# Kernel tuning notes

Measured on AMD Instinct MI355X. Metric: run time of the kernel, lower is better.

The kernel has to match this reference:

```python
import jax, jax.numpy as jnp
import numpy as np

N_INST = 50000
D_IN, D_HID, D_ATT = 1024, 512, 256  # size_dict['small']
N_ENS = 4
N_CLS = 2
CB_SIZE = 256
BETA = 0.25
TOP_K = 1


def setup_inputs() -> dict:
    key = jax.random.key(0)
    ks = jax.random.split(key, 9)
    h = jax.random.normal(ks[0], (N_INST, D_IN), dtype=jnp.float32)
    fc_W = jax.random.normal(ks[1], (D_IN, D_HID), dtype=jnp.float32) * (1.0 / np.sqrt(D_IN))
    fc_b = jnp.zeros((D_HID,), dtype=jnp.float32)
    Ua = jax.random.normal(ks[2], (N_ENS, D_HID, D_ATT), dtype=jnp.float32) * (1.0 / np.sqrt(D_HID))
    Ub = jax.random.normal(ks[3], (N_ENS, D_HID, D_ATT), dtype=jnp.float32) * (1.0 / np.sqrt(D_HID))
    Uc = jax.random.normal(ks[4], (N_ENS, D_ATT, 1), dtype=jnp.float32) * (1.0 / np.sqrt(D_ATT))
    cls_W = jax.random.normal(ks[5], (D_HID, N_CLS), dtype=jnp.float32) * (1.0 / np.sqrt(D_HID))
    cls_b = jnp.zeros((N_CLS,), dtype=jnp.float32)
    codebook = jax.random.normal(ks[6], (CB_SIZE, D_HID), dtype=jnp.float32)
    return {"h": h, "fc_W": fc_W, "fc_b": fc_b, "Ua": Ua, "Ub": Ub,
            "Uc": Uc, "cls_W": cls_W, "cls_b": cls_b, "codebook": codebook}


def _vector_quantization(M, codebook):
    # NOTE: original code uses +2*matmul (sign bug in torch source); kept faithful.
    dist = (jnp.sum(M * M, axis=1, keepdims=True)
            + jnp.sum(codebook * codebook, axis=1)
            + 2.0 * (M @ codebook.T))                      # [1, CB]
    inds = jnp.argmin(dist, axis=1)                        # [1]
    one_hot = jax.nn.one_hot(inds, CB_SIZE, dtype=M.dtype)  # [1, CB]
    q = one_hot @ codebook                                  # [1, D_HID]
    commitment = jnp.mean((jax.lax.stop_gradient(q) - M) ** 2)
    embedding = jnp.mean((q - jax.lax.stop_gradient(M)) ** 2)
    vq_loss = commitment * BETA + embedding
    q_st = M + jax.lax.stop_gradient(q - M)  # straight-through (unused downstream)
    return vq_loss, q_st


def reference(h, fc_W, fc_b, Ua, Ub, Uc, cls_W, cls_b, codebook):
    # fc + ReLU: [n, D_HID]
    x = jax.nn.relu(h @ fc_W + fc_b)
    # gated batch-ensemble attention (ensemble dim n=4 broadcast)
    xe = jnp.broadcast_to(x[None], (N_ENS, x.shape[0], D_HID))
    a = jnp.tanh(jnp.einsum('ndk,nkl->ndl', xe, Ua))         # [4, n, D_ATT]
    b = jax.nn.sigmoid(jnp.einsum('ndk,nkl->ndl', xe, Ub))   # [4, n, D_ATT]
    A = jnp.einsum('ndk,nkl->ndl', a * b, Uc).sum(0)          # [n, 1]
    A = jax.nn.sigmoid(A.T)                                   # [1, n]
    M = (A @ x) / jnp.sum(A)                                  # [1, D_HID]
    vq_loss, _M_code = _vector_quantization(M, codebook)
    logits = M @ cls_W + cls_b                                # [1, N_CLS]
    y_probs = jax.nn.softmax(logits, axis=1)
    _, top_idx = jax.lax.top_k(y_probs[:, 1], TOP_K)          # [1]
    top_instance = logits[top_idx]                            # [1, N_CLS]
    Y_hat = jnp.argmax(top_instance, axis=1)[:, None]         # [1, 1] int
    Y_prob = jax.nn.softmax(top_instance, axis=1)
    return (top_instance, Y_prob, Y_hat, vq_loss, y_probs, A)
```

## Files before the change

### kernel.cpp

```cpp
#include <hip/hip_runtime.h>
#include <hip/hip_bf16.h>
#include <math.h>

typedef __bf16 bf16_t;
typedef __bf16 bf16x8 __attribute__((ext_vector_type(8)));
typedef __bf16 bf16x2 __attribute__((ext_vector_type(2)));
typedef float  f32x4  __attribute__((ext_vector_type(4)));

#define MINST 50000

__device__ __forceinline__ float fast_sigmoid(float x){
  return __fdividef(1.f, 1.f + __expf(-x));
}
__device__ __forceinline__ float fast_tanh(float x){
  float e = __expf(2.f*x);
  return 1.f - __fdividef(2.f, e + 1.f);
}

__global__ void prep_wt(const float* __restrict__ W, bf16_t* __restrict__ WT){
  int idx = blockIdx.x*256 + threadIdx.x;
  if (idx >= 512*1024) return;
  int n = idx >> 10, k = idx & 1023;
  WT[idx] = (bf16_t)W[k*512 + n];
}

__global__ void prep_uab(const float* __restrict__ Ua, const float* __restrict__ Ub,
                         bf16_t* __restrict__ UabT){
  int idx = blockIdx.x*256 + threadIdx.x;
  if (idx >= 2048*512) return;
  int c = idx >> 9, k = idx & 511;
  int s = c & 1, t = c >> 1;
  int n = t >> 8, l = t & 255;
  const float* src = s ? Ub : Ua;
  UabT[idx] = (bf16_t)src[(n*512 + k)*256 + l];
}

__global__ void zero_ws_k(float* __restrict__ Alogit, float* __restrict__ Mbuf){
  int i = blockIdx.x*256 + threadIdx.x;
  if (i < MINST) Alogit[i] = 0.f;
  if (i < 513)   Mbuf[i]  = 0.f;
}

template<int EPI, int K>
__global__ __launch_bounds__(256, 2)
void gemm_k(const void* __restrict__ Ap, const bf16_t* __restrict__ Bp, int M,
            const float* __restrict__ bias, bf16_t* __restrict__ Xout,
            const float* __restrict__ Uc, float* __restrict__ Alogit)
{
  __shared__ bf16_t As[128*40] __attribute__((aligned(16)));
  __shared__ bf16_t Bs[128*40] __attribute__((aligned(16)));
  const int tid  = threadIdx.x;
  const int lane = tid & 63;
  const int wid  = tid >> 6;
  const int wr   = wid >> 1;
  const int wc   = wid & 1;
  const int m0   = blockIdx.x * 128;
  const int n0   = blockIdx.y * 128;

  const f32x4 fzero = {0.f, 0.f, 0.f, 0.f};
  f32x4 acc[4][4];
#pragma unroll
  for (int m = 0; m < 4; ++m)
#pragma unroll
    for (int n = 0; n < 4; ++n) acc[m][n] = fzero;

  const int q_row  = tid >> 2;
  const int q_c    = tid & 3;
  const int a_row  = tid >> 1;
  const int a_half = tid & 1;

  bf16x8 sB0, sB1, sA0, sA1;
  f32x4  sAf[4];

  auto loadTiles = [&](int k0){
    sB0 = *(const bf16x8*)(Bp + (size_t)(n0 + q_row     )*K + k0 + q_c*8);
    sB1 = *(const bf16x8*)(Bp + (size_t)(n0 + q_row + 64)*K + k0 + q_c*8);
    if constexpr (EPI == 0) {
      const float* A = (const float*)Ap;
      int gr = m0 + a_row;
      if (gr < M) {
        const f32x4* p = (const f32x4*)(A + (size_t)gr*K + k0 + a_half*16);
        sAf[0]=p[0]; sAf[1]=p[1]; sAf[2]=p[2]; sAf[3]=p[3];
      } else {
        sAf[0]=fzero; sAf[1]=fzero; sAf[2]=fzero; sAf[3]=fzero;
      }
    } else {
      const bf16_t* A = (const bf16_t*)Ap;
      int g0 = m0 + q_row, g1 = m0 + q_row + 64;
      bf16x8 z;
#pragma unroll
      for (int j = 0; j < 8; ++j) z[j] = (bf16_t)0.f;
      sA0 = (g0 < M) ? *(const bf16x8*)(A + (size_t)g0*K + k0 + q_c*8) : z;
      sA1 = (g1 < M) ? *(const bf16x8*)(A + (size_t)g1*K + k0 + q_c*8) : z;
    }
  };

  auto storeTiles = [&](){
    *(bf16x8*)&Bs[(q_row     )*40 + q_c*8] = sB0;
    *(bf16x8*)&Bs[(q_row + 64)*40 + q_c*8] = sB1;
    if constexpr (EPI == 0) {
      bf16x8 lo, hi;
#pragma unroll
      for (int j = 0; j < 4; ++j) {
        lo[j]   = (bf16_t)sAf[0][j];
        lo[4+j] = (bf16_t)sAf[1][j];
        hi[j]   = (bf16_t)sAf[2][j];
        hi[4+j] = (bf16_t)sAf[3][j];
      }
      *(bf16x8*)&As[a_row*40 + a_half*16    ] = lo;
      *(bf16x8*)&As[a_row*40 + a_half*16 + 8] = hi;
    } else {
      *(bf16x8*)&As[(q_row     )*40 + q_c*8] = sA0;
      *(bf16x8*)&As[(q_row + 64)*40 + q_c*8] = sA1;
    }
  };

  loadTiles(0);
  const int fr = lane & 15;
  const int kh = lane >> 4;
  constexpr int NT = K / 32;
  for (int kt = 0; kt < NT; ++kt) {
    __syncthreads();
    storeTiles();
    __syncthreads();
    if (kt + 1 < NT) loadTiles((kt+1)*32);
    bf16x8 a[4], b[4];
#pragma unroll
    for (int m = 0; m < 4; ++m)
      a[m] = *(const bf16x8*)&As[(wr*64 + m*16 + fr)*40 + kh*8];
#pragma unroll
    for (int n = 0; n < 4; ++n)
      b[n] = *(const bf16x8*)&Bs[(wc*64 + n*16 + fr)*40 + kh*8];
#pragma unroll
    for (int m = 0; m < 4; ++m)
#pragma unroll
      for (int n = 0; n < 4; ++n)
        acc[m][n] = __builtin_amdgcn_mfma_f32_16x16x32_bf16(a[m], b[n], acc[m][n], 0, 0, 0);
  }

  const int rg = lane >> 4;
  if constexpr (EPI == 0) {
#pragma unroll
    for (int n = 0; n < 4; ++n) {
      int col = n0 + wc*64 + n*16 + fr;
      float bv = bias[col];
#pragma unroll
      for (int m = 0; m < 4; ++m)
#pragma unroll
        for (int r = 0; r < 4; ++r) {
          int row = m0 + wr*64 + m*16 + rg*4 + r;
          if (row < M) {
            float v = acc[m][n][r] + bv;
            Xout[(size_t)row*512 + col] = (bf16_t)(v > 0.f ? v : 0.f);
          }
        }
    }
  } else {
    float gacc[4][4];
#pragma unroll
    for (int m = 0; m < 4; ++m)
#pragma unroll
      for (int r = 0; r < 4; ++r) gacc[m][r] = 0.f;
    const bool even = (lane & 1) == 0;
#pragma unroll
    for (int n = 0; n < 4; ++n) {
      int col = n0 + wc*64 + n*16 + fr;
      float ucv = Uc[col >> 1];
#pragma unroll
      for (int m = 0; m < 4; ++m)
#pragma unroll
        for (int r = 0; r < 4; ++r) {
          float v = acc[m][n][r];
          float p = __shfl_xor(v, 1);
          float g = even ? fast_tanh(v) * fast_sigmoid(p) * ucv : 0.f;
          gacc[m][r] += g;
        }
    }
#pragma unroll
    for (int m = 0; m < 4; ++m)
#pragma unroll
      for (int r = 0; r < 4; ++r) {
        float s = gacc[m][r];
        s += __shfl_xor(s, 1);
        s += __shfl_xor(s, 2);
        s += __shfl_xor(s, 4);
        s += __shfl_xor(s, 8);
        if (fr == 0) {
          int row = m0 + wr*64 + m*16 + rg*4 + r;
          if (row < M) atomicAdd(&Alogit[row], s);
        }
      }
  }
}

__global__ void a_final(const float* __restrict__ Alogit, float* __restrict__ outA,
                        float* __restrict__ sumA){
  int i = blockIdx.x*256 + threadIdx.x;
  float a = 0.f;
  if (i < MINST) { a = fast_sigmoid(Alogit[i]); outA[i] = a; }
  float s = a;
#pragma unroll
  for (int o = 1; o < 64; o <<= 1) s += __shfl_xor(s, o);
  __shared__ float wsum[4];
  int lane = threadIdx.x & 63, w = threadIdx.x >> 6;
  if (lane == 0) wsum[w] = s;
  __syncthreads();
  if (threadIdx.x == 0) atomicAdd(sumA, wsum[0]+wsum[1]+wsum[2]+wsum[3]);
}

__global__ void m_reduce(const bf16_t* __restrict__ Xb, const float* __restrict__ Aout,
                         float* __restrict__ Mbuf){
  int t = threadIdx.x;
  int c0 = t*2;
  float acc0 = 0.f, acc1 = 0.f;
  for (int r = blockIdx.x; r < MINST; r += gridDim.x) {
    float a = Aout[r];
    bf16x2 x = *(const bf16x2*)(Xb + (size_t)r*512 + c0);
    acc0 += a * (float)x[0];
    acc1 += a * (float)x[1];
  }
  atomicAdd(&Mbuf[c0],   acc0);
  atomicAdd(&Mbuf[c0+1], acc1);
}

__device__ __forceinline__ float block_sum256(float v, float* red){
  int t = threadIdx.x;
  red[t] = v; __syncthreads();
  for (int s = 128; s > 0; s >>= 1) {
    if (t < s) red[t] += red[t+s];
    __syncthreads();
  }
  float r = red[0];
  __syncthreads();
  return r;
}

__global__ __launch_bounds__(256)
void finalize_k(const float* __restrict__ Mbuf, const float* __restrict__ cb,
                const float* __restrict__ clsW, const float* __restrict__ clsb,
                float* __restrict__ dout)
{
  __shared__ float Mn[512];
  __shared__ float red[256];
  __shared__ float dist[256];
  __shared__ int   idxs[256];
  __shared__ int   indS;
  int t = threadIdx.x;
  float sA = Mbuf[512];
  Mn[t]     = Mbuf[t]     / sA;
  Mn[t+256] = Mbuf[t+256] / sA;
  __syncthreads();
  float msq_p = Mn[t]*Mn[t] + Mn[t+256]*Mn[t+256];
  float Msq = block_sum256(msq_p, red);

  const float* cbr = cb + t*512;
  float cs = 0.f, dt = 0.f;
  for (int k = 0; k < 512; k += 4) {
    f32x4 c = *(const f32x4*)(cbr + k);
    cs += c[0]*c[0] + c[1]*c[1] + c[2]*c[2] + c[3]*c[3];
    dt += Mn[k]*c[0] + Mn[k+1]*c[1] + Mn[k+2]*c[2] + Mn[k+3]*c[3];
  }
  dist[t] = Msq + cs + 2.f*dt;
  idxs[t] = t;
  __syncthreads();
  for (int s = 128; s > 0; s >>= 1) {
    if (t < s && dist[t+s] < dist[t]) { dist[t] = dist[t+s]; idxs[t] = idxs[t+s]; }
    __syncthreads();
  }
  if (t == 0) indS = idxs[0];
  __syncthreads();

  const float* q = cb + (size_t)indS*512;
  float d0 = q[t]     - Mn[t];
  float d1 = q[t+256] - Mn[t+256];
  float vqs = block_sum256(d0*d0 + d1*d1, red);
  float vq_loss = 1.25f * (vqs / 512.f);

  float p0 = Mn[t]*clsW[t*2]   + Mn[t+256]*clsW[(t+256)*2];
  float p1 = Mn[t]*clsW[t*2+1] + Mn[t+256]*clsW[(t+256)*2+1];
  float l0 = block_sum256(p0, red);
  float l1 = block_sum256(p1, red);

  if (t == 0) {
    l0 += clsb[0]; l1 += clsb[1];
    float mx = fmaxf(l0, l1);
    float e0 = __expf(l0 - mx), e1 = __expf(l1 - mx);
    float si = e0 + e1;
    float y0 = e0 / si, y1 = e1 / si;
    int yhat = (l1 > l0) ? 1 : 0;
    dout[0] = l0; dout[1] = l1;
    dout[2] = y0; dout[3] = y1;
    dout[4] = (float)yhat;
    dout[5] = vq_loss;
    dout[6] = y0; dout[7] = y1;
  }
}

extern "C" void kernel_launch(void* const* d_in, const int* in_sizes, int n_in,
                              void* d_out, int out_size, void* d_ws, size_t ws_size,
                              hipStream_t stream) {
  const float* h    = (const float*)d_in[0];
  const float* fcW  = (const float*)d_in[1];
  const float* fcb  = (const float*)d_in[2];
  const float* Ua   = (const float*)d_in[3];
  const float* Ub   = (const float*)d_in[4];
  const float* Uc   = (const float*)d_in[5];
  const float* clsW = (const float*)d_in[6];
  const float* clsb = (const float*)d_in[7];
  const float* cbk  = (const float*)d_in[8];
  float* out = (float*)d_out;

  char* ws = (char*)d_ws;
  bf16_t* Xb     = (bf16_t*)ws;
  bf16_t* WT     = (bf16_t*)(ws + 51200000);
  bf16_t* UabT   = (bf16_t*)(ws + 52248576);
  float*  Alogit = (float*)(ws + 54345728);
  float*  Mbuf   = (float*)(ws + 54545728);

  const int M = MINST;

  prep_wt <<<2048, 256, 0, stream>>>(fcW, WT);
  prep_uab<<<4096, 256, 0, stream>>>(Ua, Ub, UabT);
  zero_ws_k<<<196, 256, 0, stream>>>(Alogit, Mbuf);

  gemm_k<0,1024><<<dim3(391, 4), 256, 0, stream>>>(h, WT, M, fcb, Xb, nullptr, nullptr);
  gemm_k<1, 512><<<dim3(391,16), 256, 0, stream>>>(Xb, UabT, M, nullptr, nullptr, Uc, Alogit);

  a_final <<<196, 256, 0, stream>>>(Alogit, out + 8, Mbuf + 512);
  m_reduce<<<256, 256, 0, stream>>>(Xb, out + 8, Mbuf);
  finalize_k<<<1, 256, 0, stream>>>(Mbuf, cbk, clsW, clsb, out);
}
```

Measured before the change: 426.0 us.

## Stage GEMM tiles via global_load_lds double buffering with XCD-aware block remap

```diff
diff --git a/kernel.cpp b/kernel.cpp
--- a/kernel.cpp
+++ b/kernel.cpp
@@ -4,10 +4,15 @@
 
 typedef __bf16 bf16_t;
 typedef __bf16 bf16x8 __attribute__((ext_vector_type(8)));
-typedef __bf16 bf16x2 __attribute__((ext_vector_type(2)));
 typedef float  f32x4  __attribute__((ext_vector_type(4)));
 
 #define MINST 50000
+
+typedef const __attribute__((address_space(1))) void* gas1_t;
+typedef __attribute__((address_space(3))) void* las3_t;
+__device__ __forceinline__ void gload16(const void* g, const void* l){
+  __builtin_amdgcn_global_load_lds((gas1_t)g, (las3_t)l, 16, 0, 0);
+}
 
 __device__ __forceinline__ float fast_sigmoid(float x){
   return __fdividef(1.f, 1.f + __expf(-x));
@@ -41,21 +46,27 @@
   if (i < 513)   Mbuf[i]  = 0.f;
 }
 
-template<int EPI, int K>
+template<int EPI, int K, int NBY>
 __global__ __launch_bounds__(256, 2)
 void gemm_k(const void* __restrict__ Ap, const bf16_t* __restrict__ Bp, int M,
             const float* __restrict__ bias, bf16_t* __restrict__ Xout,
             const float* __restrict__ Uc, float* __restrict__ Alogit)
 {
-  __shared__ bf16_t As[128*40] __attribute__((aligned(16)));
-  __shared__ bf16_t Bs[128*40] __attribute__((aligned(16)));
+  __shared__ bf16_t As[(EPI==0?1:2)][128*32] __attribute__((aligned(16)));
+  __shared__ bf16_t Bs[2][128*32] __attribute__((aligned(16)));
+
   const int tid  = threadIdx.x;
   const int lane = tid & 63;
-  const int wid  = tid >> 6;
-  const int wr   = wid >> 1;
-  const int wc   = wid & 1;
-  const int m0   = blockIdx.x * 128;
-  const int n0   = blockIdx.y * 128;
+  const int w    = tid >> 6;
+  const int wr   = w >> 1;
+  const int wc   = w & 1;
+
+  const int nwg = gridDim.x;
+  const int q = nwg >> 3, r = nwg & 7;
+  const int x = blockIdx.x & 7, pos = blockIdx.x >> 3;
+  const int logical = (x < r ? x*(q+1) : r*(q+1) + (x-r)*q) + pos;
+  const int m0 = (logical / NBY) * 128;
+  const int n0 = (logical % NBY) * 128;
 
   const f32x4 fzero = {0.f, 0.f, 0.f, 0.f};
   f32x4 acc[4][4];
@@ -64,78 +75,97 @@
 #pragma unroll
     for (int n = 0; n < 4; ++n) acc[m][n] = fzero;
 
-  const int q_row  = tid >> 2;
-  const int q_c    = tid & 3;
+  const int srow = lane >> 2;
+  const int schk = (lane & 3) * 8;
+  const bf16_t* bsrc0 = Bp + (size_t)(n0 + w*32 + srow)*K + schk;
+  const bf16_t* bsrc1 = bsrc0 + (size_t)16*K;
+
+  auto stageB = [&](int buf, int k0){
+    gload16(bsrc0 + k0, &Bs[buf][(w*32     )*32]);
+    gload16(bsrc1 + k0, &Bs[buf][(w*32 + 16)*32]);
+  };
+
+  const bf16_t* asrc0 = (const bf16_t*)Ap + (size_t)(m0 + w*32 + srow)*K + schk;
+  const bf16_t* asrc1 = asrc0 + (size_t)16*K;
+  auto stageA1 = [&](int buf, int k0){
+    gload16(asrc0 + k0, &As[buf][(w*32     )*32]);
+    gload16(asrc1 + k0, &As[buf][(w*32 + 16)*32]);
+  };
+
   const int a_row  = tid >> 1;
   const int a_half = tid & 1;
-
-  bf16x8 sB0, sB1, sA0, sA1;
-  f32x4  sAf[4];
-
-  auto loadTiles = [&](int k0){
-    sB0 = *(const bf16x8*)(Bp + (size_t)(n0 + q_row     )*K + k0 + q_c*8);
-    sB1 = *(const bf16x8*)(Bp + (size_t)(n0 + q_row + 64)*K + k0 + q_c*8);
-    if constexpr (EPI == 0) {
-      const float* A = (const float*)Ap;
-      int gr = m0 + a_row;
-      if (gr < M) {
-        const f32x4* p = (const f32x4*)(A + (size_t)gr*K + k0 + a_half*16);
-        sAf[0]=p[0]; sAf[1]=p[1]; sAf[2]=p[2]; sAf[3]=p[3];
-      } else {
-        sAf[0]=fzero; sAf[1]=fzero; sAf[2]=fzero; sAf[3]=fzero;
-      }
+  f32x4 sAf[4];
+  auto loadA0 = [&](int k0){
+    const float* A = (const float*)Ap;
+    int gr = m0 + a_row;
+    if (gr < M) {
+      const f32x4* p = (const f32x4*)(A + (size_t)gr*K + k0 + a_half*16);
+      sAf[0]=p[0]; sAf[1]=p[1]; sAf[2]=p[2]; sAf[3]=p[3];
     } else {
-      const bf16_t* A = (const bf16_t*)Ap;
-      int g0 = m0 + q_row, g1 = m0 + q_row + 64;
-      bf16x8 z;
-#pragma unroll
-      for (int j = 0; j < 8; ++j) z[j] = (bf16_t)0.f;
-      sA0 = (g0 < M) ? *(const bf16x8*)(A + (size_t)g0*K + k0 + q_c*8) : z;
-      sA1 = (g1 < M) ? *(const bf16x8*)(A + (size_t)g1*K + k0 + q_c*8) : z;
+      sAf[0]=fzero; sAf[1]=fzero; sAf[2]=fzero; sAf[3]=fzero;
     }
   };
-
-  auto storeTiles = [&](){
-    *(bf16x8*)&Bs[(q_row     )*40 + q_c*8] = sB0;
-    *(bf16x8*)&Bs[(q_row + 64)*40 + q_c*8] = sB1;
-    if constexpr (EPI == 0) {
-      bf16x8 lo, hi;
-#pragma unroll
-      for (int j = 0; j < 4; ++j) {
-        lo[j]   = (bf16_t)sAf[0][j];
-        lo[4+j] = (bf16_t)sAf[1][j];
-        hi[j]   = (bf16_t)sAf[2][j];
-        hi[4+j] = (bf16_t)sAf[3][j];
-      }
-      *(bf16x8*)&As[a_row*40 + a_half*16    ] = lo;
-      *(bf16x8*)&As[a_row*40 + a_half*16 + 8] = hi;
-    } else {
-      *(bf16x8*)&As[(q_row     )*40 + q_c*8] = sA0;
-      *(bf16x8*)&As[(q_row + 64)*40 + q_c*8] = sA1;
-    }
+  auto writeA0 = [&](){
+    bf16x8 lo, hi;
+#pragma unroll
+    for (int j = 0; j < 4; ++j) {
+      lo[j]   = (bf16_t)sAf[0][j];
+      lo[4+j] = (bf16_t)sAf[1][j];
+      hi[j]   = (bf16_t)sAf[2][j];
+      hi[4+j] = (bf16_t)sAf[3][j];
+    }
+    *(bf16x8*)&As[0][a_row*32 + a_half*16    ] = lo;
+    *(bf16x8*)&As[0][a_row*32 + a_half*16 + 8] = hi;
   };
 
-  loadTiles(0);
   const int fr = lane & 15;
   const int kh = lane >> 4;
   constexpr int NT = K / 32;
-  for (int kt = 0; kt < NT; ++kt) {
-    __syncthreads();
-    storeTiles();
-    __syncthreads();
-    if (kt + 1 < NT) loadTiles((kt+1)*32);
-    bf16x8 a[4], b[4];
-#pragma unroll
-    for (int m = 0; m < 4; ++m)
-      a[m] = *(const bf16x8*)&As[(wr*64 + m*16 + fr)*40 + kh*8];
-#pragma unroll
-    for (int n = 0; n < 4; ++n)
-      b[n] = *(const bf16x8*)&Bs[(wc*64 + n*16 + fr)*40 + kh*8];
-#pragma unroll
-    for (int m = 0; m < 4; ++m)
+
+  if constexpr (EPI == 0) {
+    loadA0(0);
+    stageB(0, 0);
+#pragma unroll 4
+    for (int kt = 0; kt < NT; ++kt) {
+      const int cur = kt & 1;
+      __syncthreads();
+      writeA0();
+      __syncthreads();
+      if (kt + 1 < NT) { loadA0((kt+1)*32); stageB(cur^1, (kt+1)*32); }
+      bf16x8 a[4], b[4];
+#pragma unroll
+      for (int m = 0; m < 4; ++m)
+        a[m] = *(const bf16x8*)&As[0][(wr*64 + m*16 + fr)*32 + kh*8];
 #pragma unroll
       for (int n = 0; n < 4; ++n)
-        acc[m][n] = __builtin_amdgcn_mfma_f32_16x16x32_bf16(a[m], b[n], acc[m][n], 0, 0, 0);
+        b[n] = *(const bf16x8*)&Bs[cur][(wc*64 + n*16 + fr)*32 + kh*8];
+#pragma unroll
+      for (int m = 0; m < 4; ++m)
+#pragma unroll
+        for (int n = 0; n < 4; ++n)
+          acc[m][n] = __builtin_amdgcn_mfma_f32_16x16x32_bf16(a[m], b[n], acc[m][n], 0, 0, 0);
+    }
+  } else {
+    stageA1(0, 0);
+    stageB(0, 0);
+#pragma unroll 4
+    for (int kt = 0; kt < NT; ++kt) {
+      const int cur = kt & 1;
+      __syncthreads();
+      if (kt + 1 < NT) { stageA1(cur^1, (kt+1)*32); stageB(cur^1, (kt+1)*32); }
+      bf16x8 a[4], b[4];
+#pragma unroll
+      for (int m = 0; m < 4; ++m)
+        a[m] = *(const bf16x8*)&As[cur][(wr*64 + m*16 + fr)*32 + kh*8];
+#pragma unroll
+      for (int n = 0; n < 4; ++n)
+        b[n] = *(const bf16x8*)&Bs[cur][(wc*64 + n*16 + fr)*32 + kh*8];
+#pragma unroll
+      for (int m = 0; m < 4; ++m)
+#pragma unroll
+        for (int n = 0; n < 4; ++n)
+          acc[m][n] = __builtin_amdgcn_mfma_f32_16x16x32_bf16(a[m], b[n], acc[m][n], 0, 0, 0);
+    }
   }
 
   const int rg = lane >> 4;
@@ -147,10 +177,10 @@
 #pragma unroll
       for (int m = 0; m < 4; ++m)
 #pragma unroll
-        for (int r = 0; r < 4; ++r) {
-          int row = m0 + wr*64 + m*16 + rg*4 + r;
+        for (int rr = 0; rr < 4; ++rr) {
+          int row = m0 + wr*64 + m*16 + rg*4 + rr;
           if (row < M) {
-            float v = acc[m][n][r] + bv;
+            float v = acc[m][n][rr] + bv;
             Xout[(size_t)row*512 + col] = (bf16_t)(v > 0.f ? v : 0.f);
           }
         }
@@ -160,7 +190,7 @@
 #pragma unroll
     for (int m = 0; m < 4; ++m)
 #pragma unroll
-      for (int r = 0; r < 4; ++r) gacc[m][r] = 0.f;
+      for (int rr = 0; rr < 4; ++rr) gacc[m][rr] = 0.f;
     const bool even = (lane & 1) == 0;
 #pragma unroll
     for (int n = 0; n < 4; ++n) {
@@ -169,25 +199,25 @@
 #pragma unroll
       for (int m = 0; m < 4; ++m)
 #pragma unroll
-        for (int r = 0; r < 4; ++r) {
-          float v = acc[m][n][r];
-          float p = __shfl_xor(v, 1);
-          float g = even ? fast_tanh(v) * fast_sigmoid(p) * ucv : 0.f;
-          gacc[m][r] += g;
+        for (int rr = 0; rr < 4; ++rr) {
+          float v = acc[m][n][rr];
+          float tv = even ? fast_tanh(v) : fast_sigmoid(v);
+          float pv = __shfl_xor(tv, 1);
+          gacc[m][rr] += tv * pv * ucv;
         }
     }
 #pragma unroll
     for (int m = 0; m < 4; ++m)
 #pragma unroll
-      for (int r = 0; r < 4; ++r) {
-        float s = gacc[m][r];
+      for (int rr = 0; rr < 4; ++rr) {
+        float s = gacc[m][rr];
         s += __shfl_xor(s, 1);
         s += __shfl_xor(s, 2);
         s += __shfl_xor(s, 4);
         s += __shfl_xor(s, 8);
         if (fr == 0) {
-          int row = m0 + wr*64 + m*16 + rg*4 + r;
-          if (row < M) atomicAdd(&Alogit[row], s);
+          int row = m0 + wr*64 + m*16 + rg*4 + rr;
+          if (row < M) atomicAdd(&Alogit[row], 0.5f * s);
         }
       }
   }
@@ -211,16 +241,18 @@
 __global__ void m_reduce(const bf16_t* __restrict__ Xb, const float* __restrict__ Aout,
                          float* __restrict__ Mbuf){
   int t = threadIdx.x;
-  int c0 = t*2;
-  float acc0 = 0.f, acc1 = 0.f;
-  for (int r = blockIdx.x; r < MINST; r += gridDim.x) {
+  int c0 = (t & 63) * 8;
+  float acc[8];
+#pragma unroll
+  for (int j = 0; j < 8; ++j) acc[j] = 0.f;
+  for (int r = blockIdx.x*4 + (t>>6); r < MINST; r += gridDim.x*4) {
     float a = Aout[r];
-    bf16x2 x = *(const bf16x2*)(Xb + (size_t)r*512 + c0);
-    acc0 += a * (float)x[0];
-    acc1 += a * (float)x[1];
-  }
-  atomicAdd(&Mbuf[c0],   acc0);
-  atomicAdd(&Mbuf[c0+1], acc1);
+    bf16x8 xv = *(const bf16x8*)(Xb + (size_t)r*512 + c0);
+#pragma unroll
+    for (int j = 0; j < 8; ++j) acc[j] += a * (float)xv[j];
+  }
+#pragma unroll
+  for (int j = 0; j < 8; ++j) atomicAdd(&Mbuf[c0 + j], acc[j]);
 }
 
 __device__ __forceinline__ float block_sum256(float v, float* red){
@@ -230,9 +262,9 @@
     if (t < s) red[t] += red[t+s];
     __syncthreads();
   }
-  float r = red[0];
-  __syncthreads();
-  return r;
+  float rr = red[0];
+  __syncthreads();
+  return rr;
 }
 
 __global__ __launch_bounds__(256)
@@ -270,9 +302,9 @@
   if (t == 0) indS = idxs[0];
   __syncthreads();
 
-  const float* q = cb + (size_t)indS*512;
-  float d0 = q[t]     - Mn[t];
-  float d1 = q[t+256] - Mn[t+256];
+  const float* qv = cb + (size_t)indS*512;
+  float d0 = qv[t]     - Mn[t];
+  float d1 = qv[t+256] - Mn[t+256];
   float vqs = block_sum256(d0*d0 + d1*d1, red);
   float vq_loss = 1.25f * (vqs / 512.f);
 
@@ -323,10 +355,10 @@
   prep_uab<<<4096, 256, 0, stream>>>(Ua, Ub, UabT);
   zero_ws_k<<<196, 256, 0, stream>>>(Alogit, Mbuf);
 
-  gemm_k<0,1024><<<dim3(391, 4), 256, 0, stream>>>(h, WT, M, fcb, Xb, nullptr, nullptr);
-  gemm_k<1, 512><<<dim3(391,16), 256, 0, stream>>>(Xb, UabT, M, nullptr, nullptr, Uc, Alogit);
+  gemm_k<0,1024,4><<<1564, 256, 0, stream>>>(h, WT, M, fcb, Xb, nullptr, nullptr);
+  gemm_k<1, 512,16><<<6256, 256, 0, stream>>>(Xb, UabT, M, nullptr, nullptr, Uc, Alogit);
 
   a_final <<<196, 256, 0, stream>>>(Alogit, out + 8, Mbuf + 512);
-  m_reduce<<<256, 256, 0, stream>>>(Xb, out + 8, Mbuf);
+  m_reduce<<<128, 256, 0, stream>>>(Xb, out + 8, Mbuf);
   finalize_k<<<1, 256, 0, stream>>>(Mbuf, cbk, clsW, clsb, out);
 }
```

New measurement: 507.1 us. +19.0%, slower.
